# Performance work log

Hardware: AMD Instinct MI355X
Metric: run time of the kernel (lower is better)

## Reference

```python
import jax, jax.numpy as jnp
import numpy as np

N_NODES = 50000


def gcn_conv(x, edge_index, W, b, n_nodes):
    """PyG GCNConv: add self-loops, symmetric deg normalization, gather-scatter."""
    src, dst = edge_index[0], edge_index[1]
    loop = jnp.arange(n_nodes, dtype=src.dtype)
    src = jnp.concatenate([src, loop])
    dst = jnp.concatenate([dst, loop])
    # transform first (in -> hidden), then propagate
    h = x @ W  # [N, H]
    ones = jnp.ones_like(dst, dtype=h.dtype)
    deg = jax.ops.segment_sum(ones, dst, num_segments=n_nodes)  # [N]
    dinv = jnp.where(deg > 0, jax.lax.rsqrt(deg), 0.0)
    norm = dinv[src] * dinv[dst]  # [E+N]
    msg = h[src] * norm[:, None]  # [E+N, H] gather + scale
    out = jax.ops.segment_sum(msg, dst, num_segments=n_nodes)  # scatter-add
    return out + b


def setup_inputs() -> dict:
    key = jax.random.key(0)
    ks = jax.random.split(key, 5)
    N, E, C_in, H, C_out = N_NODES, 800000, 128, 128, 1
    x = jax.random.normal(ks[0], (N, C_in), dtype=jnp.float32)
    edge_index = jax.random.randint(ks[1], (2, E), 0, N, dtype=jnp.int32)
    sc_in = 1.0 / np.sqrt(C_in)
    sc_h = 1.0 / np.sqrt(H)
    W_gcn = jax.random.normal(ks[2], (C_in, H), dtype=jnp.float32) * sc_in
    b_gcn = jnp.zeros((H,), dtype=jnp.float32)
    W1 = jax.random.normal(ks[3], (H, H), dtype=jnp.float32) * sc_h
    b1 = jnp.zeros((H,), dtype=jnp.float32)
    W2 = jax.random.normal(ks[4], (H, C_out), dtype=jnp.float32) * sc_h
    b2 = jnp.zeros((C_out,), dtype=jnp.float32)
    return {"x": x, "edge_index": edge_index, "W_gcn": W_gcn, "b_gcn": b_gcn,
            "W1": W1, "b1": b1, "W2": W2, "b2": b2}


def reference(x, edge_index, W_gcn, b_gcn, W1, b1, W2, b2):
    n_nodes = x.shape[0]
    h = jax.nn.relu(gcn_conv(x, edge_index, W_gcn, b_gcn, n_nodes))
    h = jax.nn.relu(h @ W1 + b1)
    return h @ W2 + b2
```

## Files before the change

kernel.cpp:

```cpp
#include <hip/hip_runtime.h>
#include <hip/hip_bf16.h>

#define HID 128
#define EPB 2048
#define CAP 2560
#define NBMAX 400

typedef __attribute__((ext_vector_type(8))) short bf16x8;
typedef __attribute__((ext_vector_type(4))) float f32x4;

static inline size_t align256(size_t x) { return (x + 255) & ~(size_t)255; }

__device__ __forceinline__ unsigned short f2bf(float f) {
    unsigned int u = __float_as_uint(f);
    unsigned int r = (u + 0x7fffu + ((u >> 16) & 1u)) >> 16;
    return (unsigned short)r;
}
__device__ __forceinline__ float2 bf2x2(unsigned int u) {
    return make_float2(__uint_as_float(u << 16), __uint_as_float(u & 0xffff0000u));
}

__global__ void k_prep(const float* __restrict__ W, const float* __restrict__ W1,
                       unsigned short* __restrict__ WT, unsigned short* __restrict__ W1T,
                       int* __restrict__ gbase, int nbuck) {
    int idx = blockIdx.x * 256 + threadIdx.x;
    if (idx < HID * HID) {
        int k = idx >> 7, n = idx & 127;
        WT[n * HID + k]  = f2bf(W[idx]);
        W1T[n * HID + k] = f2bf(W1[idx]);
    }
    if (idx < nbuck) gbase[idx] = idx * CAP;
}

__global__ __launch_bounds__(256) void k_gemm_bin(
        const float* __restrict__ x, const unsigned short* __restrict__ WT,
        unsigned short* __restrict__ hs, int N,
        const int* __restrict__ src, const int* __restrict__ dst, int E,
        int* __restrict__ gbase, unsigned int* __restrict__ ebuf,
        int nbuck, int gemm_blocks) {
    __shared__ int sh_h[NBMAX], sh_cur[NBMAX];
    int bid = blockIdx.x;
    if (bid < gemm_blocks) {
        int tid = threadIdx.x;
        int wid = tid >> 6, lane = tid & 63;
        int m = lane & 15, q = lane >> 4;
        int row0 = bid * 64 + wid * 16;
        int arow_i = row0 + m;
        bool rvalid = arow_i < N;
        const float* arow = x + (size_t)arow_i * HID;
        f32x4 acc[8];
#pragma unroll
        for (int t = 0; t < 8; t++) acc[t] = (f32x4){0.f, 0.f, 0.f, 0.f};
#pragma unroll
        for (int c = 0; c < 4; c++) {
            bf16x8 a;
            if (rvalid) {
                float4 f0 = *(const float4*)(arow + c * 32 + q * 8);
                float4 f1 = *(const float4*)(arow + c * 32 + q * 8 + 4);
                a = (bf16x8){(short)f2bf(f0.x), (short)f2bf(f0.y), (short)f2bf(f0.z), (short)f2bf(f0.w),
                             (short)f2bf(f1.x), (short)f2bf(f1.y), (short)f2bf(f1.z), (short)f2bf(f1.w)};
            } else {
                a = (bf16x8){0, 0, 0, 0, 0, 0, 0, 0};
            }
#pragma unroll
            for (int t = 0; t < 8; t++) {
                bf16x8 b = *(const bf16x8*)(WT + (size_t)(t * 16 + m) * HID + c * 32 + q * 8);
                acc[t] = __builtin_amdgcn_mfma_f32_16x16x32_bf16(a, b, acc[t], 0, 0, 0);
            }
        }
#pragma unroll
        for (int t = 0; t < 8; t++) {
#pragma unroll
            for (int r = 0; r < 4; r++) {
                int rr = row0 + q * 4 + r;
                if (rr < N) hs[(size_t)rr * HID + t * 16 + m] = f2bf(acc[t][r]);
            }
        }
        return;
    }
    int blk = bid - gemm_blocks;
    int t = threadIdx.x;
    for (int i = t; i < nbuck; i += 256) sh_h[i] = 0;
    __syncthreads();
    int e0 = blk * EPB;
    bool full = (e0 + EPB <= E);
    int s[8], d[8];
    if (full) {
        int4 sa = ((const int4*)(src + e0))[t * 2];
        int4 sb = ((const int4*)(src + e0))[t * 2 + 1];
        int4 da = ((const int4*)(dst + e0))[t * 2];
        int4 db = ((const int4*)(dst + e0))[t * 2 + 1];
        s[0] = sa.x; s[1] = sa.y; s[2] = sa.z; s[3] = sa.w;
        s[4] = sb.x; s[5] = sb.y; s[6] = sb.z; s[7] = sb.w;
        d[0] = da.x; d[1] = da.y; d[2] = da.z; d[3] = da.w;
        d[4] = db.x; d[5] = db.y; d[6] = db.z; d[7] = db.w;
    } else {
#pragma unroll
        for (int i = 0; i < 8; i++) {
            int e = e0 + t * 8 + i;
            s[i] = (e < E) ? src[e] : 0;
            d[i] = (e < E) ? dst[e] : 0;
        }
    }
#pragma unroll
    for (int i = 0; i < 8; i++) {
        int e = e0 + t * 8 + i;
        if (e < E) atomicAdd(&sh_h[d[i] >> 7], 1);
    }
    __syncthreads();
    for (int i = t; i < nbuck; i += 256) {
        int v = sh_h[i];
        if (v) sh_cur[i] = atomicAdd(&gbase[i], v);
    }
    __syncthreads();
#pragma unroll
    for (int i = 0; i < 8; i++) {
        int e = e0 + t * 8 + i;
        if (e < E) {
            int b = d[i] >> 7;
            int p = atomicAdd(&sh_cur[b], 1);
            ebuf[p] = (unsigned int)s[i] | ((unsigned int)d[i] << 16);
        }
    }
}

__global__ __launch_bounds__(256) void k_bsort(const unsigned int* __restrict__ ebuf,
                                               const int* __restrict__ gbase,
                                               unsigned short* __restrict__ esorted,
                                               int* __restrict__ rs, int* __restrict__ re,
                                               float* __restrict__ dinv, int N) {
    __shared__ int cnt[128], cur[128];
    int k = blockIdx.x, t = threadIdx.x;
    int node0 = k << 7;
    int e0 = k * CAP;
    int e1 = gbase[k];
    if (t < 128) cnt[t] = 0;
    __syncthreads();
    unsigned int u[10];
#pragma unroll
    for (int i = 0; i < 10; i++) {
        int e = e0 + t + i * 256;
        u[i] = (e < e1) ? ebuf[e] : 0xffffffffu;
    }
#pragma unroll
    for (int i = 0; i < 10; i++)
        if (u[i] != 0xffffffffu) atomicAdd(&cnt[(u[i] >> 16) & 127u], 1);
    __syncthreads();
    if (t < 64) {
        int carry = 0;
#pragma unroll
        for (int c = 0; c < 2; c++) {
            int n = c * 64 + t;
            int v = cnt[n];
            int sc = v;
            for (int off = 1; off < 64; off <<= 1) {
                int w = __shfl_up(sc, off);
                if (t >= off) sc += w;
            }
            int excl = carry + (sc - v);
            cur[n] = e0 + excl;
            int node = node0 + n;
            if (node < N) {
                rs[node] = e0 + excl;
                re[node] = e0 + excl + v;
                dinv[node] = rsqrtf((float)(v + 1));
            }
            carry += __shfl(sc, 63);
        }
    }
    __syncthreads();
#pragma unroll
    for (int i = 0; i < 10; i++) {
        if (u[i] != 0xffffffffu) {
            int n = (int)((u[i] >> 16) & 127u);
            int pos = atomicAdd(&cur[n], 1);
            esorted[pos] = (unsigned short)(u[i] & 0xffffu);
        }
    }
}

__global__ __launch_bounds__(256) void k_prop(const unsigned short* __restrict__ hs,
                       const int* __restrict__ rs, const int* __restrict__ re,
                       const unsigned short* __restrict__ esorted, const float* __restrict__ dinv,
                       const float* __restrict__ b_gcn,
                       unsigned short* __restrict__ out1, int N) {
    int wave = blockIdx.x * 4 + (threadIdx.x >> 6);
    int nwaves = gridDim.x * 4;
    int lane = threadIdx.x & 63;
    int g = lane >> 4;
    int fl = lane & 15;
    const uint4* hsv = (const uint4*)hs;
    float4 b0 = *(const float4*)(b_gcn + fl * 8);
    float4 b1 = *(const float4*)(b_gcn + fl * 8 + 4);
    for (int node = wave; node < N; node += nwaves) {
        int s0 = rs[node], s1 = re[node];
        float di = dinv[node];
        float a0 = 0.f, a1 = 0.f, a2 = 0.f, a3 = 0.f, a4 = 0.f, a5 = 0.f, a6 = 0.f, a7 = 0.f;
        int j = s0;
        for (; j + 16 <= s1; j += 16) {
            int eA = esorted[j + g], eB = esorted[j + 4 + g];
            int eC = esorted[j + 8 + g], eD = esorted[j + 12 + g];
            float dA = dinv[eA], dB = dinv[eB], dC = dinv[eC], dD = dinv[eD];
            uint4 uA = hsv[(size_t)eA * 16 + fl];
            uint4 uB = hsv[(size_t)eB * 16 + fl];
            uint4 uC = hsv[(size_t)eC * 16 + fl];
            uint4 uD = hsv[(size_t)eD * 16 + fl];
            float2 f;
            f = bf2x2(uA.x); a0 += dA * f.x; a1 += dA * f.y;
            f = bf2x2(uA.y); a2 += dA * f.x; a3 += dA * f.y;
            f = bf2x2(uA.z); a4 += dA * f.x; a5 += dA * f.y;
            f = bf2x2(uA.w); a6 += dA * f.x; a7 += dA * f.y;
            f = bf2x2(uB.x); a0 += dB * f.x; a1 += dB * f.y;
            f = bf2x2(uB.y); a2 += dB * f.x; a3 += dB * f.y;
            f = bf2x2(uB.z); a4 += dB * f.x; a5 += dB * f.y;
            f = bf2x2(uB.w); a6 += dB * f.x; a7 += dB * f.y;
            f = bf2x2(uC.x); a0 += dC * f.x; a1 += dC * f.y;
            f = bf2x2(uC.y); a2 += dC * f.x; a3 += dC * f.y;
            f = bf2x2(uC.z); a4 += dC * f.x; a5 += dC * f.y;
            f = bf2x2(uC.w); a6 += dC * f.x; a7 += dC * f.y;
            f = bf2x2(uD.x); a0 += dD * f.x; a1 += dD * f.y;
            f = bf2x2(uD.y); a2 += dD * f.x; a3 += dD * f.y;
            f = bf2x2(uD.z); a4 += dD * f.x; a5 += dD * f.y;
            f = bf2x2(uD.w); a6 += dD * f.x; a7 += dD * f.y;
        }
        for (; j + 8 <= s1; j += 8) {
            int eA = esorted[j + g], eB = esorted[j + 4 + g];
            float dA = dinv[eA], dB = dinv[eB];
            uint4 uA = hsv[(size_t)eA * 16 + fl];
            uint4 uB = hsv[(size_t)eB * 16 + fl];
            float2 f;
            f = bf2x2(uA.x); a0 += dA * f.x; a1 += dA * f.y;
            f = bf2x2(uA.y); a2 += dA * f.x; a3 += dA * f.y;
            f = bf2x2(uA.z); a4 += dA * f.x; a5 += dA * f.y;
            f = bf2x2(uA.w); a6 += dA * f.x; a7 += dA * f.y;
            f = bf2x2(uB.x); a0 += dB * f.x; a1 += dB * f.y;
            f = bf2x2(uB.y); a2 += dB * f.x; a3 += dB * f.y;
            f = bf2x2(uB.z); a4 += dB * f.x; a5 += dB * f.y;
            f = bf2x2(uB.w); a6 += dB * f.x; a7 += dB * f.y;
        }
        for (; j + g < s1; j += 4) {
            int ei = esorted[j + g];
            float dA = dinv[ei];
            uint4 u = hsv[(size_t)ei * 16 + fl];
            float2 f;
            f = bf2x2(u.x); a0 += dA * f.x; a1 += dA * f.y;
            f = bf2x2(u.y); a2 += dA * f.x; a3 += dA * f.y;
            f = bf2x2(u.z); a4 += dA * f.x; a5 += dA * f.y;
            f = bf2x2(u.w); a6 += dA * f.x; a7 += dA * f.y;
        }
        if (g == 0) {
            uint4 u = hsv[(size_t)node * 16 + fl];
            float2 f;
            f = bf2x2(u.x); a0 += di * f.x; a1 += di * f.y;
            f = bf2x2(u.y); a2 += di * f.x; a3 += di * f.y;
            f = bf2x2(u.z); a4 += di * f.x; a5 += di * f.y;
            f = bf2x2(u.w); a6 += di * f.x; a7 += di * f.y;
        }
#pragma unroll
        for (int off = 16; off <= 32; off <<= 1) {
            a0 += __shfl_xor(a0, off); a1 += __shfl_xor(a1, off);
            a2 += __shfl_xor(a2, off); a3 += __shfl_xor(a3, off);
            a4 += __shfl_xor(a4, off); a5 += __shfl_xor(a5, off);
            a6 += __shfl_xor(a6, off); a7 += __shfl_xor(a7, off);
        }
        if (g == 0) {
            uint4 o;
            o.x = (unsigned int)f2bf(fmaxf(di * a0 + b0.x, 0.f)) | ((unsigned int)f2bf(fmaxf(di * a1 + b0.y, 0.f)) << 16);
            o.y = (unsigned int)f2bf(fmaxf(di * a2 + b0.z, 0.f)) | ((unsigned int)f2bf(fmaxf(di * a3 + b0.w, 0.f)) << 16);
            o.z = (unsigned int)f2bf(fmaxf(di * a4 + b1.x, 0.f)) | ((unsigned int)f2bf(fmaxf(di * a5 + b1.y, 0.f)) << 16);
            o.w = (unsigned int)f2bf(fmaxf(di * a6 + b1.z, 0.f)) | ((unsigned int)f2bf(fmaxf(di * a7 + b1.w, 0.f)) << 16);
            ((uint4*)out1)[(size_t)node * 16 + fl] = o;
        }
    }
}

__global__ __launch_bounds__(256) void k_mlp(const unsigned short* __restrict__ out1,
                                             const unsigned short* __restrict__ W1T,
                                             const float* __restrict__ b1,
                                             const float* __restrict__ W2,
                                             const float* __restrict__ b2,
                                             float* __restrict__ out, int N) {
    __shared__ float sb1[128], sW2[128];
    int tid = threadIdx.x;
    if (tid < 128) { sb1[tid] = b1[tid]; sW2[tid] = W2[tid]; }
    __syncthreads();
    int wid = tid >> 6, lane = tid & 63;
    int m = lane & 15, q = lane >> 4;
    int row0 = blockIdx.x * 64 + wid * 16;
    int arow_i = row0 + m;
    bool rvalid = arow_i < N;
    const unsigned short* arow = out1 + (size_t)arow_i * HID;
    f32x4 acc[8];
#pragma unroll
    for (int t = 0; t < 8; t++) acc[t] = (f32x4){0.f, 0.f, 0.f, 0.f};
#pragma unroll
    for (int c = 0; c < 4; c++) {
        bf16x8 a = rvalid ? *(const bf16x8*)(arow + c * 32 + q * 8)
                          : (bf16x8){0, 0, 0, 0, 0, 0, 0, 0};
#pragma unroll
        for (int t = 0; t < 8; t++) {
            bf16x8 b = *(const bf16x8*)(W1T + (size_t)(t * 16 + m) * HID + c * 32 + q * 8);
            acc[t] = __builtin_amdgcn_mfma_f32_16x16x32_bf16(a, b, acc[t], 0, 0, 0);
        }
    }
    float part[4] = {0.f, 0.f, 0.f, 0.f};
#pragma unroll
    for (int t = 0; t < 8; t++) {
        int nc = t * 16 + m;
        float w2 = sW2[nc], bb = sb1[nc];
#pragma unroll
        for (int r = 0; r < 4; r++)
            part[r] += fmaxf(acc[t][r] + bb, 0.f) * w2;
    }
#pragma unroll
    for (int off = 8; off >= 1; off >>= 1) {
#pragma unroll
        for (int r = 0; r < 4; r++) part[r] += __shfl_xor(part[r], off);
    }
    if (m == 0) {
        float bb = b2[0];
#pragma unroll
        for (int r = 0; r < 4; r++) {
            int rr = row0 + q * 4 + r;
            if (rr < N) out[rr] = part[r] + bb;
        }
    }
}

extern "C" void kernel_launch(void* const* d_in, const int* in_sizes, int n_in,
                              void* d_out, int out_size, void* d_ws, size_t ws_size,
                              hipStream_t stream) {
    const float* x     = (const float*)d_in[0];
    const int*   ei    = (const int*)d_in[1];
    const float* W_gcn = (const float*)d_in[2];
    const float* b_gcn = (const float*)d_in[3];
    const float* W1    = (const float*)d_in[4];
    const float* b1    = (const float*)d_in[5];
    const float* W2    = (const float*)d_in[6];
    const float* b2    = (const float*)d_in[7];
    float* out = (float*)d_out;

    int N = in_sizes[0] / HID;
    int E = in_sizes[1] / 2;
    const int* e_src = ei;
    const int* e_dst = ei + E;
    int NBUCK = (N + 127) >> 7;
    int NBLK = (E + EPB - 1) / EPB;

    char* ws = (char*)d_ws;
    size_t off = 0;
    unsigned short* hs = (unsigned short*)(ws + off);      off = align256(off + (size_t)N * HID * 2);
    unsigned short* out1 = (unsigned short*)(ws + off);    off = align256(off + (size_t)N * HID * 2);
    float* dinv = (float*)(ws + off);                      off = align256(off + (size_t)N * 4);
    int* rs = (int*)(ws + off);                            off = align256(off + (size_t)N * 4);
    int* re = (int*)(ws + off);                            off = align256(off + (size_t)N * 4);
    int* gbase = (int*)(ws + off);                         off = align256(off + (size_t)NBUCK * 4);
    unsigned int* ebuf = (unsigned int*)(ws + off);        off = align256(off + (size_t)NBUCK * CAP * 4);
    unsigned short* esorted = (unsigned short*)(ws + off); off = align256(off + (size_t)NBUCK * CAP * 2);
    unsigned short* WT = (unsigned short*)(ws + off);      off = align256(off + (size_t)HID * HID * 2);
    unsigned short* W1T = (unsigned short*)(ws + off);     off = align256(off + (size_t)HID * HID * 2);

    int mfma_blocks = (N + 63) / 64;

    k_prep<<<(HID * HID + 255) / 256, 256, 0, stream>>>(W_gcn, W1, WT, W1T, gbase, NBUCK);

    k_gemm_bin<<<mfma_blocks + NBLK, 256, 0, stream>>>(x, WT, hs, N, e_src, e_dst, E,
                                                       gbase, ebuf, NBUCK, mfma_blocks);

    k_bsort<<<NBUCK, 256, 0, stream>>>(ebuf, gbase, esorted, rs, re, dinv, N);

    k_prop<<<2048, 256, 0, stream>>>(hs, rs, re, esorted, dinv, b_gcn, out1, N);

    k_mlp<<<mfma_blocks, 256, 0, stream>>>(out1, W1T, b1, W2, b2, out, N);
}
```

Measured before the change: 163.6 us.

## Fuse bucket sort, propagation and MLP into one per-bucket kernel

Shrinks the buckets to 64 nodes and merges the per-bucket sort, the gather-aggregate and the MLP into one kernel. Each block sorts its bucket's edges in shared memory and stages the aggregated hidden rows in LDS, then runs the MFMA MLP directly from there. This removes the esorted/out1/rs/re/dinv round trips and two launches. Degrees now come from global atomics during binning, and dinv is recomputed with rsqrt on every neighbor access. Propagation parallelism drops to one block per 64 nodes.

```diff
diff --git a/kernel.cpp b/kernel.cpp
--- a/kernel.cpp
+++ b/kernel.cpp
@@ -3,8 +3,10 @@
 
 #define HID 128
 #define EPB 2048
-#define CAP 2560
-#define NBMAX 400
+#define BSH 6
+#define CAP 1280
+#define NBMAX 800
+#define SROW 136
 
 typedef __attribute__((ext_vector_type(8))) short bf16x8;
 typedef __attribute__((ext_vector_type(4))) float f32x4;
@@ -16,19 +18,23 @@
     unsigned int r = (u + 0x7fffu + ((u >> 16) & 1u)) >> 16;
     return (unsigned short)r;
 }
+__device__ __forceinline__ float bf2f(unsigned short h) {
+    return __uint_as_float(((unsigned int)h) << 16);
+}
 __device__ __forceinline__ float2 bf2x2(unsigned int u) {
     return make_float2(__uint_as_float(u << 16), __uint_as_float(u & 0xffff0000u));
 }
 
 __global__ void k_prep(const float* __restrict__ W, const float* __restrict__ W1,
                        unsigned short* __restrict__ WT, unsigned short* __restrict__ W1T,
-                       int* __restrict__ gbase, int nbuck) {
+                       int* __restrict__ deg, int* __restrict__ gbase, int N, int nbuck) {
     int idx = blockIdx.x * 256 + threadIdx.x;
     if (idx < HID * HID) {
         int k = idx >> 7, n = idx & 127;
         WT[n * HID + k]  = f2bf(W[idx]);
         W1T[n * HID + k] = f2bf(W1[idx]);
     }
+    if (idx < N) deg[idx] = 0;
     if (idx < nbuck) gbase[idx] = idx * CAP;
 }
 
@@ -37,7 +43,7 @@
         unsigned short* __restrict__ hs, int N,
         const int* __restrict__ src, const int* __restrict__ dst, int E,
         int* __restrict__ gbase, unsigned int* __restrict__ ebuf,
-        int nbuck, int gemm_blocks) {
+        int* __restrict__ deg, int nbuck, int gemm_blocks) {
     __shared__ int sh_h[NBMAX], sh_cur[NBMAX];
     int bid = blockIdx.x;
     if (bid < gemm_blocks) {
@@ -105,7 +111,10 @@
 #pragma unroll
     for (int i = 0; i < 8; i++) {
         int e = e0 + t * 8 + i;
-        if (e < E) atomicAdd(&sh_h[d[i] >> 7], 1);
+        if (e < E) {
+            atomicAdd(&sh_h[d[i] >> BSH], 1);
+            atomicAdd(&deg[d[i]], 1);
+        }
     }
     __syncthreads();
     for (int i = t; i < nbuck; i += 256) {
@@ -117,90 +126,87 @@
     for (int i = 0; i < 8; i++) {
         int e = e0 + t * 8 + i;
         if (e < E) {
-            int b = d[i] >> 7;
+            int b = d[i] >> BSH;
             int p = atomicAdd(&sh_cur[b], 1);
             ebuf[p] = (unsigned int)s[i] | ((unsigned int)d[i] << 16);
         }
     }
 }
 
-__global__ __launch_bounds__(256) void k_bsort(const unsigned int* __restrict__ ebuf,
-                                               const int* __restrict__ gbase,
-                                               unsigned short* __restrict__ esorted,
-                                               int* __restrict__ rs, int* __restrict__ re,
-                                               float* __restrict__ dinv, int N) {
-    __shared__ int cnt[128], cur[128];
-    int k = blockIdx.x, t = threadIdx.x;
-    int node0 = k << 7;
-    int e0 = k * CAP;
-    int e1 = gbase[k];
-    if (t < 128) cnt[t] = 0;
-    __syncthreads();
-    unsigned int u[10];
-#pragma unroll
-    for (int i = 0; i < 10; i++) {
-        int e = e0 + t + i * 256;
-        u[i] = (e < e1) ? ebuf[e] : 0xffffffffu;
-    }
-#pragma unroll
-    for (int i = 0; i < 10; i++)
-        if (u[i] != 0xffffffffu) atomicAdd(&cnt[(u[i] >> 16) & 127u], 1);
-    __syncthreads();
-    if (t < 64) {
-        int carry = 0;
-#pragma unroll
-        for (int c = 0; c < 2; c++) {
-            int n = c * 64 + t;
-            int v = cnt[n];
-            int sc = v;
-            for (int off = 1; off < 64; off <<= 1) {
-                int w = __shfl_up(sc, off);
-                if (t >= off) sc += w;
-            }
-            int excl = carry + (sc - v);
-            cur[n] = e0 + excl;
-            int node = node0 + n;
-            if (node < N) {
-                rs[node] = e0 + excl;
-                re[node] = e0 + excl + v;
-                dinv[node] = rsqrtf((float)(v + 1));
-            }
-            carry += __shfl(sc, 63);
-        }
-    }
-    __syncthreads();
-#pragma unroll
-    for (int i = 0; i < 10; i++) {
-        if (u[i] != 0xffffffffu) {
-            int n = (int)((u[i] >> 16) & 127u);
-            int pos = atomicAdd(&cur[n], 1);
-            esorted[pos] = (unsigned short)(u[i] & 0xffffu);
-        }
-    }
-}
-
-__global__ __launch_bounds__(256) void k_prop(const unsigned short* __restrict__ hs,
-                       const int* __restrict__ rs, const int* __restrict__ re,
-                       const unsigned short* __restrict__ esorted, const float* __restrict__ dinv,
-                       const float* __restrict__ b_gcn,
-                       unsigned short* __restrict__ out1, int N) {
-    int wave = blockIdx.x * 4 + (threadIdx.x >> 6);
-    int nwaves = gridDim.x * 4;
-    int lane = threadIdx.x & 63;
+__global__ __launch_bounds__(256) void k_prop_mlp(
+        const unsigned short* __restrict__ hs,
+        const unsigned int* __restrict__ ebuf, const int* __restrict__ gbase,
+        const int* __restrict__ deg,
+        const float* __restrict__ b_gcn,
+        const unsigned short* __restrict__ W1T,
+        const float* __restrict__ b1, const float* __restrict__ W2,
+        const float* __restrict__ b2,
+        float* __restrict__ out, int N) {
+    __shared__ int sE[CAP];
+    __shared__ int scnt[64], scur[64], srow0[64];
+    __shared__ __align__(16) unsigned short stage[64 * SROW];
+    __shared__ float sb1[128], sW2[128];
+    int k = blockIdx.x, tid = threadIdx.x;
+    int node0 = k << BSH;
+    int wid = tid >> 6, lane = tid & 63;
     int g = lane >> 4;
     int fl = lane & 15;
+
+    if (tid < 64) scnt[tid] = 0;
+    if (tid < 128) { sb1[tid] = b1[tid]; sW2[tid] = W2[tid]; }
+    __syncthreads();
+
+    int e0 = k * CAP, e1 = gbase[k];
+    unsigned int ue[5];
+#pragma unroll
+    for (int i = 0; i < 5; i++) {
+        int e = e0 + tid + i * 256;
+        ue[i] = (e < e1) ? ebuf[e] : 0xffffffffu;
+    }
+#pragma unroll
+    for (int i = 0; i < 5; i++)
+        if (ue[i] != 0xffffffffu) atomicAdd(&scnt[(ue[i] >> 16) & 63u], 1);
+    __syncthreads();
+    if (tid < 64) {
+        int v = scnt[tid];
+        int sc = v;
+#pragma unroll
+        for (int off = 1; off < 64; off <<= 1) {
+            int u = __shfl_up(sc, off);
+            if (tid >= off) sc += u;
+        }
+        int excl = sc - v;
+        scur[tid] = excl;
+        srow0[tid] = excl;
+    }
+    __syncthreads();
+#pragma unroll
+    for (int i = 0; i < 5; i++) {
+        if (ue[i] != 0xffffffffu) {
+            int r = (int)((ue[i] >> 16) & 63u);
+            int pos = atomicAdd(&scur[r], 1);
+            sE[pos] = (int)(ue[i] & 0xffffu);
+        }
+    }
+    __syncthreads();
+
     const uint4* hsv = (const uint4*)hs;
     float4 b0 = *(const float4*)(b_gcn + fl * 8);
-    float4 b1 = *(const float4*)(b_gcn + fl * 8 + 4);
-    for (int node = wave; node < N; node += nwaves) {
-        int s0 = rs[node], s1 = re[node];
-        float di = dinv[node];
+    float4 b1v = *(const float4*)(b_gcn + fl * 8 + 4);
+    for (int r = wid * 16; r < wid * 16 + 16; r++) {
+        int s0 = srow0[r], s1 = scur[r];
+        int node = node0 + r;
+        bool rv = node < N;
+        float di = rv ? rsqrtf((float)deg[node] + 1.0f) : 0.f;
         float a0 = 0.f, a1 = 0.f, a2 = 0.f, a3 = 0.f, a4 = 0.f, a5 = 0.f, a6 = 0.f, a7 = 0.f;
         int j = s0;
         for (; j + 16 <= s1; j += 16) {
-            int eA = esorted[j + g], eB = esorted[j + 4 + g];
-            int eC = esorted[j + 8 + g], eD = esorted[j + 12 + g];
-            float dA = dinv[eA], dB = dinv[eB], dC = dinv[eC], dD = dinv[eD];
+            int eA = sE[j + g], eB = sE[j + 4 + g];
+            int eC = sE[j + 8 + g], eD = sE[j + 12 + g];
+            float dA = rsqrtf((float)deg[eA] + 1.f);
+            float dB = rsqrtf((float)deg[eB] + 1.f);
+            float dC = rsqrtf((float)deg[eC] + 1.f);
+            float dD = rsqrtf((float)deg[eD] + 1.f);
             uint4 uA = hsv[(size_t)eA * 16 + fl];
             uint4 uB = hsv[(size_t)eB * 16 + fl];
             uint4 uC = hsv[(size_t)eC * 16 + fl];
@@ -224,8 +230,9 @@
             f = bf2x2(uD.w); a6 += dD * f.x; a7 += dD * f.y;
         }
         for (; j + 8 <= s1; j += 8) {
-            int eA = esorted[j + g], eB = esorted[j + 4 + g];
-            float dA = dinv[eA], dB = dinv[eB];
+            int eA = sE[j + g], eB = sE[j + 4 + g];
+            float dA = rsqrtf((float)deg[eA] + 1.f);
+            float dB = rsqrtf((float)deg[eB] + 1.f);
             uint4 uA = hsv[(size_t)eA * 16 + fl];
             uint4 uB = hsv[(size_t)eB * 16 + fl];
             float2 f;
@@ -239,8 +246,8 @@
             f = bf2x2(uB.w); a6 += dB * f.x; a7 += dB * f.y;
         }
         for (; j + g < s1; j += 4) {
-            int ei = esorted[j + g];
-            float dA = dinv[ei];
+            int ei = sE[j + g];
+            float dA = rsqrtf((float)deg[ei] + 1.f);
             uint4 u = hsv[(size_t)ei * 16 + fl];
             float2 f;
             f = bf2x2(u.x); a0 += dA * f.x; a1 += dA * f.y;
@@ -248,7 +255,7 @@
             f = bf2x2(u.z); a4 += dA * f.x; a5 += dA * f.y;
             f = bf2x2(u.w); a6 += dA * f.x; a7 += dA * f.y;
         }
-        if (g == 0) {
+        if (g == 0 && rv) {
             uint4 u = hsv[(size_t)node * 16 + fl];
             float2 f;
             f = bf2x2(u.x); a0 += di * f.x; a1 += di * f.y;
@@ -267,36 +274,20 @@
             uint4 o;
             o.x = (unsigned int)f2bf(fmaxf(di * a0 + b0.x, 0.f)) | ((unsigned int)f2bf(fmaxf(di * a1 + b0.y, 0.f)) << 16);
             o.y = (unsigned int)f2bf(fmaxf(di * a2 + b0.z, 0.f)) | ((unsigned int)f2bf(fmaxf(di * a3 + b0.w, 0.f)) << 16);
-            o.z = (unsigned int)f2bf(fmaxf(di * a4 + b1.x, 0.f)) | ((unsigned int)f2bf(fmaxf(di * a5 + b1.y, 0.f)) << 16);
-            o.w = (unsigned int)f2bf(fmaxf(di * a6 + b1.z, 0.f)) | ((unsigned int)f2bf(fmaxf(di * a7 + b1.w, 0.f)) << 16);
-            ((uint4*)out1)[(size_t)node * 16 + fl] = o;
-        }
-    }
-}
-
-__global__ __launch_bounds__(256) void k_mlp(const unsigned short* __restrict__ out1,
-                                             const unsigned short* __restrict__ W1T,
-                                             const float* __restrict__ b1,
-                                             const float* __restrict__ W2,
-                                             const float* __restrict__ b2,
-                                             float* __restrict__ out, int N) {
-    __shared__ float sb1[128], sW2[128];
-    int tid = threadIdx.x;
-    if (tid < 128) { sb1[tid] = b1[tid]; sW2[tid] = W2[tid]; }
-    __syncthreads();
-    int wid = tid >> 6, lane = tid & 63;
+            o.z = (unsigned int)f2bf(fmaxf(di * a4 + b1v.x, 0.f)) | ((unsigned int)f2bf(fmaxf(di * a5 + b1v.y, 0.f)) << 16);
+            o.w = (unsigned int)f2bf(fmaxf(di * a6 + b1v.z, 0.f)) | ((unsigned int)f2bf(fmaxf(di * a7 + b1v.w, 0.f)) << 16);
+            *(uint4*)(stage + r * SROW + fl * 8) = o;
+        }
+    }
+
     int m = lane & 15, q = lane >> 4;
-    int row0 = blockIdx.x * 64 + wid * 16;
-    int arow_i = row0 + m;
-    bool rvalid = arow_i < N;
-    const unsigned short* arow = out1 + (size_t)arow_i * HID;
+    int row = wid * 16 + m;
     f32x4 acc[8];
 #pragma unroll
     for (int t = 0; t < 8; t++) acc[t] = (f32x4){0.f, 0.f, 0.f, 0.f};
 #pragma unroll
     for (int c = 0; c < 4; c++) {
-        bf16x8 a = rvalid ? *(const bf16x8*)(arow + c * 32 + q * 8)
-                          : (bf16x8){0, 0, 0, 0, 0, 0, 0, 0};
+        bf16x8 a = *(const bf16x8*)(stage + row * SROW + c * 32 + q * 8);
 #pragma unroll
         for (int t = 0; t < 8; t++) {
             bf16x8 b = *(const bf16x8*)(W1T + (size_t)(t * 16 + m) * HID + c * 32 + q * 8);
@@ -309,20 +300,20 @@
         int nc = t * 16 + m;
         float w2 = sW2[nc], bb = sb1[nc];
 #pragma unroll
-        for (int r = 0; r < 4; r++)
-            part[r] += fmaxf(acc[t][r] + bb, 0.f) * w2;
+        for (int r2 = 0; r2 < 4; r2++)
+            part[r2] += fmaxf(acc[t][r2] + bb, 0.f) * w2;
     }
 #pragma unroll
     for (int off = 8; off >= 1; off >>= 1) {
 #pragma unroll
-        for (int r = 0; r < 4; r++) part[r] += __shfl_xor(part[r], off);
+        for (int r2 = 0; r2 < 4; r2++) part[r2] += __shfl_xor(part[r2], off);
     }
     if (m == 0) {
         float bb = b2[0];
 #pragma unroll
-        for (int r = 0; r < 4; r++) {
-            int rr = row0 + q * 4 + r;
-            if (rr < N) out[rr] = part[r] + bb;
+        for (int r2 = 0; r2 < 4; r2++) {
+            int rr = node0 + wid * 16 + q * 4 + r2;
+            if (rr < N) out[rr] = part[r2] + bb;
         }
     }
 }
@@ -344,32 +335,24 @@
     int E = in_sizes[1] / 2;
     const int* e_src = ei;
     const int* e_dst = ei + E;
-    int NBUCK = (N + 127) >> 7;
+    int NBUCK = (N + 63) >> BSH;
     int NBLK = (E + EPB - 1) / EPB;
 
     char* ws = (char*)d_ws;
     size_t off = 0;
     unsigned short* hs = (unsigned short*)(ws + off);      off = align256(off + (size_t)N * HID * 2);
-    unsigned short* out1 = (unsigned short*)(ws + off);    off = align256(off + (size_t)N * HID * 2);
-    float* dinv = (float*)(ws + off);                      off = align256(off + (size_t)N * 4);
-    int* rs = (int*)(ws + off);                            off = align256(off + (size_t)N * 4);
-    int* re = (int*)(ws + off);                            off = align256(off + (size_t)N * 4);
+    int* deg = (int*)(ws + off);                           off = align256(off + (size_t)N * 4);
     int* gbase = (int*)(ws + off);                         off = align256(off + (size_t)NBUCK * 4);
     unsigned int* ebuf = (unsigned int*)(ws + off);        off = align256(off + (size_t)NBUCK * CAP * 4);
-    unsigned short* esorted = (unsigned short*)(ws + off); off = align256(off + (size_t)NBUCK * CAP * 2);
     unsigned short* WT = (unsigned short*)(ws + off);      off = align256(off + (size_t)HID * HID * 2);
     unsigned short* W1T = (unsigned short*)(ws + off);     off = align256(off + (size_t)HID * HID * 2);
 
     int mfma_blocks = (N + 63) / 64;
 
-    k_prep<<<(HID * HID + 255) / 256, 256, 0, stream>>>(W_gcn, W1, WT, W1T, gbase, NBUCK);
+    k_prep<<<(N + 255) / 256, 256, 0, stream>>>(W_gcn, W1, WT, W1T, deg, gbase, N, NBUCK);
 
     k_gemm_bin<<<mfma_blocks + NBLK, 256, 0, stream>>>(x, WT, hs, N, e_src, e_dst, E,
-                                                       gbase, ebuf, NBUCK, mfma_blocks);
-
-    k_bsort<<<NBUCK, 256, 0, stream>>>(ebuf, gbase, esorted, rs, re, dinv, N);
-
-    k_prop<<<2048, 256, 0, stream>>>(hs, rs, re, esorted, dinv, b_gcn, out1, N);
-
-    k_mlp<<<mfma_blocks, 256, 0, stream>>>(out1, W1T, b1, W2, b2, out, N);
-}
+                                                       gbase, ebuf, deg, NBUCK, mfma_blocks);
+
+    k_prop_mlp<<<NBUCK, 256, 0, stream>>>(hs, ebuf, gbase, deg, b_gcn, W1T, b1, W2, b2, out, N);
+}
```

After: 188.4 us. 15.2% more time.
